# Performance work log

Measured on AMD Instinct MI355X. Metric: run time of the kernel, lower is better.

## Reference

```python
import jax, jax.numpy as jnp
import numpy as np

WIN = 9  # 9x9 local attention window

def conv2d(x, w, b=None, pad=1):
    # x: [B,C,H,W], w: [O,I,kh,kw]
    y = jax.lax.conv_general_dilated(x, w, (1, 1), [(pad, pad), (pad, pad)],
                                     dimension_numbers=('NCHW', 'OIHW', 'NCHW'))
    if b is not None:
        y = y + b[None, :, None, None]
    return y

def leaky(x):
    return jax.nn.leaky_relu(x, 0.2)

def local_similar(q, k):
    # TorchLocalAttention.f_similar: per-pixel dot(q[i,j], k[i+di-4, j+dj-4]) with zero pad,
    # kernel positions row-major (di*9+dj) -> output [B, 81, H, W]
    b, c, h, w = q.shape
    r = WIN // 2
    kp = jnp.pad(k, ((0, 0), (0, 0), (r, r), (r, r)))
    sims = []
    for di in range(WIN):
        for dj in range(WIN):
            sims.append(jnp.einsum('bchw,bchw->bhw', q, kp[:, :, di:di + h, dj:dj + w]))
    return jnp.stack(sims, axis=1)

def srp_forward(old, new, wq, bq, wk, bk, wv, bv, wo1, bo1, res_w1, res_w2, wo2, bo2):
    x = jnp.concatenate((old, new), axis=1)  # [B, C, H, W]
    att = local_similar(conv2d(x, wq, bq), conv2d(x, wk, bk))  # [B, 81, H, W]
    v = conv2d(att, wv, bv)  # [B, C, H, W]
    y = conv2d(x * v, wo1, bo1)
    n_res = res_w1.shape[0]
    for i in range(n_res):  # EBlock: ResBlocks (convs bias=False)
        h1 = leaky(conv2d(y, res_w1[i]))
        y = y + conv2d(h1, res_w2[i])
    y = conv2d(y, wo2, bo2)
    return y + x

def setup_inputs() -> dict:
    key = jax.random.key(0)
    B, Cn, Co, H, W = 4, 32, 32, 256, 256
    C = Cn + Co
    NRES = 8
    ks = jax.random.split(key, 16)
    s = 0.05
    inp = {
        'old': jax.random.normal(ks[0], (B, Co, H, W), jnp.float32),
        'new': jax.random.normal(ks[1], (B, Cn, H, W), jnp.float32),
        'wq': jax.random.normal(ks[2], (C, C, 3, 3), jnp.float32) * s,
        'bq': jax.random.normal(ks[3], (C,), jnp.float32) * s,
        'wk': jax.random.normal(ks[4], (C, C, 3, 3), jnp.float32) * s,
        'bk': jax.random.normal(ks[5], (C,), jnp.float32) * s,
        'wv': jax.random.normal(ks[6], (C, 81, 3, 3), jnp.float32) * s,
        'bv': jax.random.normal(ks[7], (C,), jnp.float32) * s,
        'wo1': jax.random.normal(ks[8], (C, C, 3, 3), jnp.float32) * s,
        'bo1': jax.random.normal(ks[9], (C,), jnp.float32) * s,
        'res_w1': jax.random.normal(ks[10], (NRES, C, C, 3, 3), jnp.float32) * s,
        'res_w2': jax.random.normal(ks[11], (NRES, C, C, 3, 3), jnp.float32) * s,
        'wo2': jax.random.normal(ks[12], (C, C, 3, 3), jnp.float32) * s,
        'bo2': jax.random.normal(ks[13], (C,), jnp.float32) * s,
    }
    return inp

def reference(old, new, wq, bq, wk, bk, wv, bv, wo1, bo1, res_w1, res_w2, wo2, bo2):
    return srp_forward(old, new, wq, bq, wk, bk, wv, bv, wo1, bo1, res_w1, res_w2, wo2, bo2)
```

## Files before the change

### kernel.cpp

```cpp
#include <hip/hip_runtime.h>
#include <hip/hip_bf16.h>


#define HH 256
#define WW 256
#define PLANE 65536

typedef _Float16 f16x8 __attribute__((ext_vector_type(8)));
typedef float    f32x4 __attribute__((ext_vector_type(4)));
typedef _Float16 h2    __attribute__((ext_vector_type(2)));

__device__ __forceinline__ unsigned short f2h(float f) {
    _Float16 h = (_Float16)f;
    return __builtin_bit_cast(unsigned short, h);
}
__device__ __forceinline__ float h2f(unsigned short u) {
    return (float)__builtin_bit_cast(_Float16, u);
}
__device__ __forceinline__ unsigned pack2h(float a, float b) {
    return (unsigned)f2h(a) | ((unsigned)f2h(b) << 16);
}
__device__ __forceinline__ float dot2h(unsigned a, unsigned b, float c) {
#if __has_builtin(__builtin_amdgcn_fdot2)
    return __builtin_amdgcn_fdot2(__builtin_bit_cast(h2, a),
                                  __builtin_bit_cast(h2, b), c, false);
#else
    h2 av = __builtin_bit_cast(h2, a), bv = __builtin_bit_cast(h2, b);
    return fmaf((float)av.x, (float)bv.x, fmaf((float)av.y, (float)bv.y, c));
#endif
}

__device__ __forceinline__ void gl16(const unsigned short* g, unsigned short* l) {
    __builtin_amdgcn_global_load_lds(
        (const __attribute__((address_space(1))) unsigned int*)(g),
        (__attribute__((address_space(3))) unsigned int*)(l),
        16, 0, 0);
}

template <int CIN, bool BIAS, bool LEAKY, bool ADDF, bool ADDX, bool MULX, bool OUTF, bool OUTB>
__global__ __launch_bounds__(256, 2) void conv_mfma(
    const unsigned short* __restrict__ in_pc,
    const unsigned short* __restrict__ wb,
    const float* __restrict__ bias,
    const unsigned short* __restrict__ addh,
    const unsigned short* __restrict__ xh,
    float* __restrict__ outf,
    unsigned short* __restrict__ outb)
{
    __shared__ unsigned short smem[39168];
    unsigned short* lds_w = smem + 20736;

    const int tid = threadIdx.x;
    const int w   = tid >> 6;
    const int ln  = tid & 63;
    const int m   = ln & 15;
    const int q   = ln >> 4;
    const int b   = blockIdx.z;
    const int tx0 = blockIdx.x * 16, ty0 = blockIdx.y * 16;
    const size_t pixb = (size_t)b * PLANE;
    const bool interior = (blockIdx.x >= 1) && (blockIdx.x <= 14) &&
                          (blockIdx.y >= 1) && (blockIdx.y <= 14);

    auto stage_in = [&](int c2s, unsigned short* dst) {
        if (interior) {
            const unsigned short* inb =
                in_pc + (pixb + (size_t)(ty0 - 1) * 256 + (tx0 - 1)) * CIN + c2s * 32;
#pragma unroll
            for (int it = 0; it < 5; ++it) {
                int u = it * 256 + tid;
                int pix = u >> 2, ps = u & 3;
                int part = ps ^ (pix & 3);
                int hy = pix / 18, hx = pix - hy * 18;
                gl16(inb + ((size_t)hy * 256 + hx) * CIN + part * 8,
                     &dst[(it * 256 + (tid & 192)) * 8]);
            }
            if (tid < 16) {
                int u = 1280 + tid;
                int pix = u >> 2, ps = u & 3;
                int part = ps ^ (pix & 3);
                int hy = pix / 18, hx = pix - hy * 18;
                gl16(inb + ((size_t)hy * 256 + hx) * CIN + part * 8,
                     &dst[1280 * 8]);
            }
        } else {
            for (int u = tid; u < 1296; u += 256) {
                int pix = u >> 2, part = u & 3;
                int hy = pix / 18, hx = pix - hy * 18;
                int gy = ty0 + hy - 1, gx = tx0 + hx - 1;
                uint4 val = make_uint4(0u, 0u, 0u, 0u);
                if ((unsigned)gy < 256u && (unsigned)gx < 256u)
                    val = *reinterpret_cast<const uint4*>(
                        in_pc + ((pixb + (size_t)gy * 256 + gx) * CIN + c2s * 32 + part * 8));
                *reinterpret_cast<uint4*>(&dst[pix * 32 + ((part ^ (pix & 3)) * 8)]) = val;
            }
        }
    };
    auto stage_w = [&](int c2s) {
        const int oc = tid >> 2, ps = tid & 3;
        const int part = ps ^ (oc & 3);
        const unsigned short* wsrc = wb + (size_t)oc * CIN + c2s * 32 + part * 8;
#pragma unroll
        for (int t = 0; t < 9; ++t)
            gl16(wsrc + (size_t)t * 64 * CIN,
                 &lds_w[t * 2048 + (tid & 192) * 8]);
    };

    f32x4 acc[4][4];
#pragma unroll
    for (int g = 0; g < 4; ++g)
#pragma unroll
        for (int p = 0; p < 4; ++p) acc[g][p] = (f32x4)0.f;

    constexpr int NC = CIN / 32;

    stage_in(0, smem);
    stage_w(0);
    __syncthreads();

    for (int c2 = 0; c2 < NC; ++c2) {
        unsigned short* cbuf = (c2 & 1) ? smem + 10368 : smem;
        if (c2 + 1 < NC)
            stage_in(c2 + 1, ((c2 + 1) & 1) ? smem + 10368 : smem);

#pragma unroll
        for (int t = 0; t < 9; ++t) {
            const int dy = t / 3, dx = t - dy * 3;
            f16x8 av[4], bv[4];
#pragma unroll
            for (int g = 0; g < 4; ++g) {
                int oc = g * 16 + m;
                av[g] = *reinterpret_cast<const f16x8*>(
                    &lds_w[t * 2048 + oc * 32 + ((q ^ (oc & 3)) * 8)]);
            }
#pragma unroll
            for (int p = 0; p < 4; ++p) {
                int hp = (w * 4 + p + dy) * 18 + m + dx;
                bv[p] = *reinterpret_cast<const f16x8*>(
                    &cbuf[hp * 32 + ((q ^ (hp & 3)) * 8)]);
            }
#pragma unroll
            for (int g = 0; g < 4; ++g)
#pragma unroll
                for (int p = 0; p < 4; ++p)
                    acc[g][p] = __builtin_amdgcn_mfma_f32_16x16x32_f16(
                        av[g], bv[p], acc[g][p], 0, 0, 0);
        }

        if (c2 + 1 < NC) {
            __syncthreads();
            stage_w(c2 + 1);
            __syncthreads();
        }
    }

    const int colx = tx0 + m;
    float4 bvec[4];
    if (BIAS) {
#pragma unroll
        for (int g = 0; g < 4; ++g)
            bvec[g] = *reinterpret_cast<const float4*>(bias + g * 16 + q * 4);
    }
    if (OUTB) __syncthreads();

#pragma unroll
    for (int g = 0; g < 4; ++g) {
#pragma unroll
        for (int p = 0; p < 4; ++p) {
            const int prow = w * 4 + p;
            const int gy   = ty0 + prow;
            const size_t pixg = pixb + (size_t)gy * 256 + colx;
            const int oc0 = g * 16 + q * 4;
            ushort4 a4, x4;
            if (ADDF) a4 = *reinterpret_cast<const ushort4*>(addh + pixg * 64 + oc0);
            if (ADDX || MULX) x4 = *reinterpret_cast<const ushort4*>(xh + pixg * 64 + oc0);
            float vals[4];
#pragma unroll
            for (int r = 0; r < 4; ++r) {
                float v = acc[g][p][r];
                if (BIAS) v += reinterpret_cast<const float*>(&bvec[g])[r];
                if (LEAKY) v = (v >= 0.f) ? v : 0.2f * v;
                if (ADDF) v += h2f(reinterpret_cast<const unsigned short*>(&a4)[r]);
                if (ADDX) v += h2f(reinterpret_cast<const unsigned short*>(&x4)[r]);
                if (MULX) v *= h2f(reinterpret_cast<const unsigned short*>(&x4)[r]);
                if (OUTF)
                    outf[((size_t)(b * 64 + oc0 + r)) * PLANE + (size_t)gy * 256 + colx] = v;
                vals[r] = v;
            }
            if (OUTB) {
                ushort4 pk;
                pk.x = f2h(vals[0]); pk.y = f2h(vals[1]);
                pk.z = f2h(vals[2]); pk.w = f2h(vals[3]);
                int pix   = prow * 16 + m;
                int part8 = g * 4 + q;
                int p16   = (part8 >> 1) ^ (pix & 7);
                *reinterpret_cast<ushort4*>(&smem[pix * 64 + p16 * 8 + (part8 & 1) * 4]) = pk;
            }
        }
    }
    if (OUTB) {
        __syncthreads();
        for (int u = tid; u < 2048; u += 256) {
            int pix = u >> 3, p16 = u & 7;
            uint4 val = *reinterpret_cast<const uint4*>(
                &smem[pix * 64 + ((p16 ^ (pix & 7)) * 8)]);
            int gy = ty0 + (pix >> 4), gx = tx0 + (pix & 15);
            *reinterpret_cast<uint4*>(
                &outb[(pixb + (size_t)gy * 256 + gx) * 64 + p16 * 8]) = val;
        }
    }
}

__global__ __launch_bounds__(256)
void local_sim(
    const unsigned short* __restrict__ qh, const unsigned short* __restrict__ kh,
    unsigned short* __restrict__ att)
{
    __shared__ unsigned short lds_k[576 * 64];

    const int tid = threadIdx.x;
    const int tx = tid & 15, ty = tid >> 4;
    const int bx = blockIdx.x * 16, by = blockIdx.y * 16;
    const int b  = blockIdx.z;
    const size_t pixb = (size_t)b * PLANE;
    const bool interior = (blockIdx.x >= 1) && (blockIdx.x <= 14) &&
                          (blockIdx.y >= 1) && (blockIdx.y <= 14);

    if (interior) {
        const unsigned short* kb =
            kh + (pixb + (size_t)(by - 4) * 256 + (bx - 4)) * 64;
#pragma unroll
        for (int it = 0; it < 18; ++it) {
            int u = it * 256 + tid;
            int pix = u >> 3, sl = u & 7;
            int part = sl ^ ((pix ^ (pix >> 3)) & 7);
            int hy = pix / 24, hx = pix - hy * 24;
            gl16(kb + ((size_t)hy * 256 + hx) * 64 + part * 8,
                 &lds_k[(it * 256 + (tid & 192)) * 8]);
        }
    } else {
        for (int u = tid; u < 4608; u += 256) {
            int pix = u >> 3, part = u & 7;
            int hy = pix / 24, hx = pix - hy * 24;
            int gy = by + hy - 4, gx = bx + hx - 4;
            uint4 val = make_uint4(0u, 0u, 0u, 0u);
            if ((unsigned)gy < 256u && (unsigned)gx < 256u)
                val = *reinterpret_cast<const uint4*>(
                    kh + ((pixb + (size_t)gy * 256 + gx) * 64 + part * 8));
            int sl = part ^ ((pix ^ (pix >> 3)) & 7);
            *reinterpret_cast<uint4*>(&lds_k[pix * 64 + sl * 8]) = val;
        }
    }
    __syncthreads();

    const unsigned short* qbase = qh + (pixb + (size_t)(by + ty) * 256 + bx + tx) * 64;
    unsigned short* op = att + (pixb + (size_t)(by + ty) * 256 + bx + tx) * 96;

    uint4 qv[8];
#pragma unroll
    for (int j = 0; j < 8; ++j)
        qv[j] = *reinterpret_cast<const uint4*>(qbase + j * 8);

#pragma unroll
    for (int g = 0; g < 3; ++g) {
        float acc[27];
#pragma unroll
        for (int i = 0; i < 27; ++i) acc[i] = 0.f;

#pragma unroll
        for (int dil = 0; dil < 3; ++dil) {
            const int hrow = (ty + g * 3 + dil) * 24 + tx;
#pragma unroll
            for (int dj = 0; dj < 9; ++dj) {
                const int hp = hrow + dj;
                const int gs = (hp ^ (hp >> 3)) & 7;
                float s = acc[dil * 9 + dj];
#pragma unroll
                for (int part = 0; part < 8; ++part) {
                    const uint4 kv = *reinterpret_cast<const uint4*>(
                        &lds_k[hp * 64 + ((part ^ gs) * 8)]);
                    s = dot2h(qv[part].x, kv.x, s);
                    s = dot2h(qv[part].y, kv.y, s);
                    s = dot2h(qv[part].z, kv.z, s);
                    s = dot2h(qv[part].w, kv.w, s);
                }
                acc[dil * 9 + dj] = s;
            }
        }

        unsigned short* o = op + g * 27;
        if (g == 0) {
            uint4 A = {pack2h(acc[0], acc[1]),  pack2h(acc[2], acc[3]),
                       pack2h(acc[4], acc[5]),  pack2h(acc[6], acc[7])};
            uint4 B = {pack2h(acc[8], acc[9]),  pack2h(acc[10], acc[11]),
                       pack2h(acc[12], acc[13]), pack2h(acc[14], acc[15])};
            uint2 C = {pack2h(acc[16], acc[17]), pack2h(acc[18], acc[19])};
            uint2 D = {pack2h(acc[20], acc[21]), pack2h(acc[22], acc[23])};
            *reinterpret_cast<uint4*>(o)      = A;
            *reinterpret_cast<uint4*>(o + 8)  = B;
            *reinterpret_cast<uint2*>(o + 16) = C;
            *reinterpret_cast<uint2*>(o + 20) = D;
            *reinterpret_cast<unsigned*>(o + 24) = pack2h(acc[24], acc[25]);
            o[26] = f2h(acc[26]);
        } else if (g == 1) {
            o[0] = f2h(acc[0]);
            *reinterpret_cast<unsigned*>(o + 1) = pack2h(acc[1], acc[2]);
            *reinterpret_cast<unsigned*>(o + 3) = pack2h(acc[3], acc[4]);
            uint4 A = {pack2h(acc[5], acc[6]),   pack2h(acc[7], acc[8]),
                       pack2h(acc[9], acc[10]),  pack2h(acc[11], acc[12])};
            uint4 B = {pack2h(acc[13], acc[14]), pack2h(acc[15], acc[16]),
                       pack2h(acc[17], acc[18]), pack2h(acc[19], acc[20])};
            *reinterpret_cast<uint4*>(o + 5)  = A;
            *reinterpret_cast<uint4*>(o + 13) = B;
            uint2 C = {pack2h(acc[21], acc[22]), pack2h(acc[23], acc[24])};
            *reinterpret_cast<uint2*>(o + 21) = C;
            *reinterpret_cast<unsigned*>(o + 25) = pack2h(acc[25], acc[26]);
        } else {
            *reinterpret_cast<unsigned*>(o) = pack2h(acc[0], acc[1]);
            uint4 A = {pack2h(acc[2], acc[3]),   pack2h(acc[4], acc[5]),
                       pack2h(acc[6], acc[7]),   pack2h(acc[8], acc[9])};
            uint4 B = {pack2h(acc[10], acc[11]), pack2h(acc[12], acc[13]),
                       pack2h(acc[14], acc[15]), pack2h(acc[16], acc[17])};
            *reinterpret_cast<uint4*>(o + 2)  = A;
            *reinterpret_cast<uint4*>(o + 10) = B;
            uint2 C = {pack2h(acc[18], acc[19]), pack2h(acc[20], acc[21])};
            *reinterpret_cast<uint2*>(o + 18) = C;
            *reinterpret_cast<unsigned*>(o + 22) = pack2h(acc[22], acc[23]);
            *reinterpret_cast<unsigned*>(o + 24) = pack2h(acc[24], acc[25]);
            o[26] = f2h(acc[26]);
        }
    }

    op[81] = 0;
    *reinterpret_cast<unsigned*>(op + 82) = 0u;
    uint2 z2 = {0u, 0u};
    uint4 z4 = {0u, 0u, 0u, 0u};
    *reinterpret_cast<uint2*>(op + 84) = z2;
    *reinterpret_cast<uint4*>(op + 88) = z4;
}

__global__ __launch_bounds__(256) void pack_x(
    const float* __restrict__ old_, const float* __restrict__ new_,
    unsigned short* __restrict__ xb)
{
    __shared__ unsigned short lds[256 * 64];
    const int tid = threadIdx.x;
    const int b = blockIdx.y;
    const size_t pixbase = (size_t)blockIdx.x * 256;
#pragma unroll
    for (int cg = 0; cg < 8; ++cg) {
        unsigned pk[4];
#pragma unroll
        for (int h = 0; h < 4; ++h) {
            int c0 = cg * 8 + h * 2;
            const float* s0 = (c0 < 32) ? old_ : new_;
            const float* s1 = ((c0 + 1) < 32) ? old_ : new_;
            float f0 = s0[((size_t)b * 32 + (c0 & 31)) * PLANE + pixbase + tid];
            float f1 = s1[((size_t)b * 32 + ((c0 + 1) & 31)) * PLANE + pixbase + tid];
            pk[h] = pack2h(f0, f1);
        }
        int p16 = cg ^ (tid & 7);
        uint4 v; v.x = pk[0]; v.y = pk[1]; v.z = pk[2]; v.w = pk[3];
        *reinterpret_cast<uint4*>(&lds[tid * 64 + p16 * 8]) = v;
    }
    __syncthreads();
    for (int r = 0; r < 8; ++r) {
        int u = r * 256 + tid;
        int pix = u >> 3, p16 = u & 7;
        uint4 v = *reinterpret_cast<const uint4*>(&lds[pix * 64 + ((p16 ^ (pix & 7)) * 8)]);
        *reinterpret_cast<uint4*>(
            &xb[((size_t)b * PLANE + pixbase + pix) * 64 + p16 * 8]) = v;
    }
}

__global__ void prep_wstd(const float* __restrict__ wq, const float* __restrict__ wk,
                          const float* __restrict__ wo1, const float* __restrict__ wo2,
                          const float* __restrict__ rw1, const float* __restrict__ rw2,
                          unsigned short* __restrict__ wstd)
{
    const int c = blockIdx.y;
    const float* src;
    if (c == 0) src = wq;
    else if (c == 1) src = wk;
    else if (c == 2) src = wo1;
    else if (c == 3) src = wo2;
    else if (c < 12) src = rw1 + (size_t)(c - 4) * 36864;
    else src = rw2 + (size_t)(c - 12) * 36864;
    int idx = blockIdx.x * 256 + threadIdx.x;
    int o = idx >> 6, i = idx & 63;
    const float* s = src + (size_t)(o * 64 + i) * 9;
    unsigned short* d = wstd + (size_t)c * 36864 + (size_t)o * 64 + i;
#pragma unroll
    for (int t = 0; t < 9; ++t) d[(size_t)t * 4096] = f2h(s[t]);
}

__global__ void prep_wv(const float* __restrict__ wv, unsigned short* __restrict__ wv96)
{
    int idx = blockIdx.x * 256 + threadIdx.x;
    int o = idx / 96, i = idx - o * 96;
    unsigned short* d = wv96 + (size_t)o * 96 + i;
    if (i < 81) {
        const float* s = wv + (size_t)(o * 81 + i) * 9;
#pragma unroll
        for (int t = 0; t < 9; ++t) d[(size_t)t * 6144] = f2h(s[t]);
    } else {
#pragma unroll
        for (int t = 0; t < 9; ++t) d[(size_t)t * 6144] = 0;
    }
}

extern "C" void kernel_launch(void* const* d_in, const int* in_sizes, int n_in,
                              void* d_out, int out_size, void* d_ws, size_t ws_size,
                              hipStream_t stream)
{
    const float* old_ = (const float*)d_in[0];
    const float* new_ = (const float*)d_in[1];
    const float* wq  = (const float*)d_in[2];  const float* bq  = (const float*)d_in[3];
    const float* wk  = (const float*)d_in[4];  const float* bk  = (const float*)d_in[5];
    const float* wv  = (const float*)d_in[6];  const float* bv  = (const float*)d_in[7];
    const float* wo1 = (const float*)d_in[8];  const float* bo1 = (const float*)d_in[9];
    const float* rw1 = (const float*)d_in[10]; const float* rw2 = (const float*)d_in[11];
    const float* wo2 = (const float*)d_in[12]; const float* bo2 = (const float*)d_in[13];
    float* out = (float*)d_out;

    char* ws = (char*)d_ws;
    unsigned short* X   = (unsigned short*)(ws);
    unsigned short* P1  = (unsigned short*)(ws + 33554432ull);
    unsigned short* P2  = (unsigned short*)(ws + 67108864ull);
    unsigned short* P3  = (unsigned short*)(ws + 100663296ull);
    unsigned short* wst = (unsigned short*)(ws + 150994944ull);
    unsigned short* wv96= (unsigned short*)(ws + 152469504ull);

    const dim3 cgrid(16, 16, 4), cblk(256);

    prep_wstd<<<dim3(16, 20), 256, 0, stream>>>(wq, wk, wo1, wo2, rw1, rw2, wst);
    prep_wv<<<dim3(24), 256, 0, stream>>>(wv, wv96);
    pack_x<<<dim3(256, 4), 256, 0, stream>>>(old_, new_, X);

    conv_mfma<64, true, false, false, false, false, false, true>
        <<<cgrid, cblk, 0, stream>>>(X, wst + 0ull * 36864, bq, nullptr, nullptr, nullptr, P1);
    conv_mfma<64, true, false, false, false, false, false, true>
        <<<cgrid, cblk, 0, stream>>>(X, wst + 1ull * 36864, bk, nullptr, nullptr, nullptr, P2);
    local_sim<<<cgrid, cblk, 0, stream>>>(P1, P2, P3);
    conv_mfma<96, true, false, false, false, true, false, true>
        <<<cgrid, cblk, 0, stream>>>(P3, wv96, bv, nullptr, X, nullptr, P2);
    conv_mfma<64, true, false, false, false, false, false, true>
        <<<cgrid, cblk, 0, stream>>>(P2, wst + 2ull * 36864, bo1, nullptr, nullptr, nullptr, P1);
    for (int i = 0; i < 8; ++i) {
        unsigned short* ysrc = (i & 1) ? P3 : P1;
        unsigned short* ydst = (i & 1) ? P1 : P3;
        conv_mfma<64, false, true, false, false, false, false, true>
            <<<cgrid, cblk, 0, stream>>>(ysrc, wst + (size_t)(4 + i) * 36864, nullptr,
                                         nullptr, nullptr, nullptr, P2);
        conv_mfma<64, false, false, true, false, false, false, true>
            <<<cgrid, cblk, 0, stream>>>(P2, wst + (size_t)(12 + i) * 36864, nullptr,
                                         ysrc, nullptr, nullptr, ydst);
    }
    conv_mfma<64, true, false, false, true, false, true, false>
        <<<cgrid, cblk, 0, stream>>>(P1, wst + 3ull * 36864, bo2, nullptr, X, out, nullptr);
}
```

Measured before the change: 833.3 us.

## Stage full 64-channel input tile once and double-buffer weights by tap pairs

For 64-input-channel convolutions, the kernel now loads the whole 18x18x64 halo tile into LDS at once with an 8-way XOR swizzle. It then streams weights in chunks of two taps through two LDS buffers, so the next chunk loads while MFMAs run on the current one. This replaces the old two-pass channel split, which needed two barriers plus a serial weight reload per pass. In exchange there are five barrier rounds per tile and a different LDS layout, and the final barrier moves inside the loop.

```diff
diff --git a/kernel.cpp b/kernel.cpp
--- a/kernel.cpp
+++ b/kernel.cpp
@@ -48,7 +48,6 @@
     unsigned short* __restrict__ outb)
 {
     __shared__ unsigned short smem[39168];
-    unsigned short* lds_w = smem + 20736;
 
     const int tid = threadIdx.x;
     const int w   = tid >> 6;
@@ -61,96 +60,189 @@
     const bool interior = (blockIdx.x >= 1) && (blockIdx.x <= 14) &&
                           (blockIdx.y >= 1) && (blockIdx.y <= 14);
 
-    auto stage_in = [&](int c2s, unsigned short* dst) {
+    f32x4 acc[4][4];
+#pragma unroll
+    for (int g = 0; g < 4; ++g)
+#pragma unroll
+        for (int p = 0; p < 4; ++p) acc[g][p] = (f32x4)0.f;
+
+    if constexpr (CIN == 64) {
+        unsigned short* lds_in = smem;
+        unsigned short* wbuf0  = smem + 20736;
+        unsigned short* wbuf1  = smem + 28928;
+
         if (interior) {
             const unsigned short* inb =
-                in_pc + (pixb + (size_t)(ty0 - 1) * 256 + (tx0 - 1)) * CIN + c2s * 32;
-#pragma unroll
-            for (int it = 0; it < 5; ++it) {
+                in_pc + (pixb + (size_t)(ty0 - 1) * 256 + (tx0 - 1)) * 64;
+#pragma unroll
+            for (int it = 0; it < 10; ++it) {
                 int u = it * 256 + tid;
-                int pix = u >> 2, ps = u & 3;
-                int part = ps ^ (pix & 3);
+                int pix = u >> 3, ps = u & 7;
+                int part = ps ^ (pix & 7);
                 int hy = pix / 18, hx = pix - hy * 18;
-                gl16(inb + ((size_t)hy * 256 + hx) * CIN + part * 8,
-                     &dst[(it * 256 + (tid & 192)) * 8]);
-            }
-            if (tid < 16) {
-                int u = 1280 + tid;
-                int pix = u >> 2, ps = u & 3;
-                int part = ps ^ (pix & 3);
+                gl16(inb + ((size_t)hy * 256 + hx) * 64 + part * 8,
+                     &lds_in[(it * 256 + (tid & 192)) * 8]);
+            }
+            if (tid < 32) {
+                int u = 2560 + tid;
+                int pix = u >> 3, ps = u & 7;
+                int part = ps ^ (pix & 7);
                 int hy = pix / 18, hx = pix - hy * 18;
-                gl16(inb + ((size_t)hy * 256 + hx) * CIN + part * 8,
-                     &dst[1280 * 8]);
+                gl16(inb + ((size_t)hy * 256 + hx) * 64 + part * 8,
+                     &lds_in[2560 * 8]);
             }
         } else {
-            for (int u = tid; u < 1296; u += 256) {
-                int pix = u >> 2, part = u & 3;
+            for (int u = tid; u < 2592; u += 256) {
+                int pix = u >> 3, part = u & 7;
                 int hy = pix / 18, hx = pix - hy * 18;
                 int gy = ty0 + hy - 1, gx = tx0 + hx - 1;
                 uint4 val = make_uint4(0u, 0u, 0u, 0u);
                 if ((unsigned)gy < 256u && (unsigned)gx < 256u)
                     val = *reinterpret_cast<const uint4*>(
-                        in_pc + ((pixb + (size_t)gy * 256 + gx) * CIN + c2s * 32 + part * 8));
-                *reinterpret_cast<uint4*>(&dst[pix * 32 + ((part ^ (pix & 3)) * 8)]) = val;
-            }
-        }
-    };
-    auto stage_w = [&](int c2s) {
-        const int oc = tid >> 2, ps = tid & 3;
-        const int part = ps ^ (oc & 3);
-        const unsigned short* wsrc = wb + (size_t)oc * CIN + c2s * 32 + part * 8;
-#pragma unroll
-        for (int t = 0; t < 9; ++t)
-            gl16(wsrc + (size_t)t * 64 * CIN,
-                 &lds_w[t * 2048 + (tid & 192) * 8]);
-    };
-
-    f32x4 acc[4][4];
-#pragma unroll
-    for (int g = 0; g < 4; ++g)
-#pragma unroll
-        for (int p = 0; p < 4; ++p) acc[g][p] = (f32x4)0.f;
-
-    constexpr int NC = CIN / 32;
-
-    stage_in(0, smem);
-    stage_w(0);
-    __syncthreads();
-
-    for (int c2 = 0; c2 < NC; ++c2) {
-        unsigned short* cbuf = (c2 & 1) ? smem + 10368 : smem;
-        if (c2 + 1 < NC)
-            stage_in(c2 + 1, ((c2 + 1) & 1) ? smem + 10368 : smem);
-
-#pragma unroll
-        for (int t = 0; t < 9; ++t) {
-            const int dy = t / 3, dx = t - dy * 3;
-            f16x8 av[4], bv[4];
-#pragma unroll
-            for (int g = 0; g < 4; ++g) {
-                int oc = g * 16 + m;
-                av[g] = *reinterpret_cast<const f16x8*>(
-                    &lds_w[t * 2048 + oc * 32 + ((q ^ (oc & 3)) * 8)]);
-            }
-#pragma unroll
-            for (int p = 0; p < 4; ++p) {
-                int hp = (w * 4 + p + dy) * 18 + m + dx;
-                bv[p] = *reinterpret_cast<const f16x8*>(
-                    &cbuf[hp * 32 + ((q ^ (hp & 3)) * 8)]);
-            }
-#pragma unroll
-            for (int g = 0; g < 4; ++g)
-#pragma unroll
-                for (int p = 0; p < 4; ++p)
-                    acc[g][p] = __builtin_amdgcn_mfma_f32_16x16x32_f16(
-                        av[g], bv[p], acc[g][p], 0, 0, 0);
-        }
-
-        if (c2 + 1 < NC) {
+                        in_pc + ((pixb + (size_t)gy * 256 + gx) * 64 + part * 8));
+                int sl = part ^ (pix & 7);
+                *reinterpret_cast<uint4*>(&lds_in[pix * 64 + sl * 8]) = val;
+            }
+        }
+
+        auto stage_w = [&](int t0, int ntaps, unsigned short* dst) {
+            for (int it = 0; it < ntaps * 2; ++it) {
+                int u = it * 256 + tid;
+                int row = u >> 3, sl = u & 7;
+                int part = sl ^ (row & 7);
+                gl16(wb + ((size_t)((t0 + (row >> 6)) * 64 + (row & 63))) * 64 + part * 8,
+                     &dst[(it * 256 + (tid & 192)) * 8]);
+            }
+        };
+
+        stage_w(0, 2, wbuf0);
+        __syncthreads();
+
+#pragma unroll
+        for (int gi = 0; gi < 5; ++gi) {
+            const int t0 = gi * 2;
+            const int nt = (gi == 4) ? 1 : 2;
+            unsigned short* cw = (gi & 1) ? wbuf1 : wbuf0;
+            if (gi < 4)
+                stage_w((gi + 1) * 2, (gi + 1 == 4) ? 1 : 2, (gi & 1) ? wbuf0 : wbuf1);
+
+#pragma unroll
+            for (int tl = 0; tl < nt; ++tl) {
+                const int t = t0 + tl;
+                const int dy = t / 3, dx = t - dy * 3;
+#pragma unroll
+                for (int c2 = 0; c2 < 2; ++c2) {
+                    f16x8 av[4], bv[4];
+#pragma unroll
+                    for (int g = 0; g < 4; ++g) {
+                        int row = tl * 64 + g * 16 + m;
+                        av[g] = *reinterpret_cast<const f16x8*>(
+                            &cw[row * 64 + (((c2 * 4 + q) ^ (m & 7)) * 8)]);
+                    }
+#pragma unroll
+                    for (int p = 0; p < 4; ++p) {
+                        int hp = (w * 4 + p + dy) * 18 + m + dx;
+                        bv[p] = *reinterpret_cast<const f16x8*>(
+                            &lds_in[hp * 64 + (((c2 * 4 + q) ^ (hp & 7)) * 8)]);
+                    }
+#pragma unroll
+                    for (int g = 0; g < 4; ++g)
+#pragma unroll
+                        for (int p = 0; p < 4; ++p)
+                            acc[g][p] = __builtin_amdgcn_mfma_f32_16x16x32_f16(
+                                av[g], bv[p], acc[g][p], 0, 0, 0);
+                }
+            }
             __syncthreads();
-            stage_w(c2 + 1);
-            __syncthreads();
-        }
+        }
+    } else {
+        unsigned short* lds_w = smem + 20736;
+
+        auto stage_in = [&](int c2s, unsigned short* dst) {
+            if (interior) {
+                const unsigned short* inb =
+                    in_pc + (pixb + (size_t)(ty0 - 1) * 256 + (tx0 - 1)) * CIN + c2s * 32;
+#pragma unroll
+                for (int it = 0; it < 5; ++it) {
+                    int u = it * 256 + tid;
+                    int pix = u >> 2, ps = u & 3;
+                    int part = ps ^ (pix & 3);
+                    int hy = pix / 18, hx = pix - hy * 18;
+                    gl16(inb + ((size_t)hy * 256 + hx) * CIN + part * 8,
+                         &dst[(it * 256 + (tid & 192)) * 8]);
+                }
+                if (tid < 16) {
+                    int u = 1280 + tid;
+                    int pix = u >> 2, ps = u & 3;
+                    int part = ps ^ (pix & 3);
+                    int hy = pix / 18, hx = pix - hy * 18;
+                    gl16(inb + ((size_t)hy * 256 + hx) * CIN + part * 8,
+                         &dst[1280 * 8]);
+                }
+            } else {
+                for (int u = tid; u < 1296; u += 256) {
+                    int pix = u >> 2, part = u & 3;
+                    int hy = pix / 18, hx = pix - hy * 18;
+                    int gy = ty0 + hy - 1, gx = tx0 + hx - 1;
+                    uint4 val = make_uint4(0u, 0u, 0u, 0u);
+                    if ((unsigned)gy < 256u && (unsigned)gx < 256u)
+                        val = *reinterpret_cast<const uint4*>(
+                            in_pc + ((pixb + (size_t)gy * 256 + gx) * CIN + c2s * 32 + part * 8));
+                    *reinterpret_cast<uint4*>(&dst[pix * 32 + ((part ^ (pix & 3)) * 8)]) = val;
+                }
+            }
+        };
+        auto stage_w = [&](int c2s) {
+            const int oc = tid >> 2, ps = tid & 3;
+            const int part = ps ^ (oc & 3);
+            const unsigned short* wsrc = wb + (size_t)oc * CIN + c2s * 32 + part * 8;
+#pragma unroll
+            for (int t = 0; t < 9; ++t)
+                gl16(wsrc + (size_t)t * 64 * CIN,
+                     &lds_w[t * 2048 + (tid & 192) * 8]);
+        };
+
+        constexpr int NC = CIN / 32;
+        stage_in(0, smem);
+        stage_w(0);
+        __syncthreads();
+
+        for (int c2 = 0; c2 < NC; ++c2) {
+            unsigned short* cbuf = (c2 & 1) ? smem + 10368 : smem;
+            if (c2 + 1 < NC)
+                stage_in(c2 + 1, ((c2 + 1) & 1) ? smem + 10368 : smem);
+
+#pragma unroll
+            for (int t = 0; t < 9; ++t) {
+                const int dy = t / 3, dx = t - dy * 3;
+                f16x8 av[4], bv[4];
+#pragma unroll
+                for (int g = 0; g < 4; ++g) {
+                    int oc = g * 16 + m;
+                    av[g] = *reinterpret_cast<const f16x8*>(
+                        &lds_w[t * 2048 + oc * 32 + ((q ^ (oc & 3)) * 8)]);
+                }
+#pragma unroll
+                for (int p = 0; p < 4; ++p) {
+                    int hp = (w * 4 + p + dy) * 18 + m + dx;
+                    bv[p] = *reinterpret_cast<const f16x8*>(
+                        &cbuf[hp * 32 + ((q ^ (hp & 3)) * 8)]);
+                }
+#pragma unroll
+                for (int g = 0; g < 4; ++g)
+#pragma unroll
+                    for (int p = 0; p < 4; ++p)
+                        acc[g][p] = __builtin_amdgcn_mfma_f32_16x16x32_f16(
+                            av[g], bv[p], acc[g][p], 0, 0, 0);
+            }
+
+            if (c2 + 1 < NC) {
+                __syncthreads();
+                stage_w(c2 + 1);
+                __syncthreads();
+            }
+        }
+        if (OUTB) __syncthreads();
     }
 
     const int colx = tx0 + m;
@@ -160,7 +252,6 @@
         for (int g = 0; g < 4; ++g)
             bvec[g] = *reinterpret_cast<const float4*>(bias + g * 16 + q * 4);
     }
-    if (OUTB) __syncthreads();
 
 #pragma unroll
     for (int g = 0; g < 4; ++g) {
```

After: 839.5 us. Within noise of the previous version (+0.7%).

## Fuse each ResBlock's two 3x3 convs into one kernel with halo recompute

Applied to the files above, without the earlier changes.

Adds a res_fused kernel that computes the first conv plus leaky ReLU on an 18x18 halo tile, keeps the intermediate in LDS, then runs the second conv and the residual add, writing y directly. The two per-ResBlock launches are replaced by one. This removes the global write and re-read of the intermediate activation and halves the launch count for the residual stack. The cost is about 27% redundant MFMA work for the halo, higher LDS use per block, and less overlap because staging is no longer double-buffered.

```diff
diff --git a/kernel.cpp b/kernel.cpp
--- a/kernel.cpp
+++ b/kernel.cpp
@@ -112,7 +112,6 @@
         for (int p = 0; p < 4; ++p) acc[g][p] = (f32x4)0.f;
 
     constexpr int NC = CIN / 32;
-
     stage_in(0, smem);
     stage_w(0);
     __syncthreads();
@@ -207,6 +206,212 @@
             *reinterpret_cast<uint4*>(
                 &outb[(pixb + (size_t)gy * 256 + gx) * 64 + p16 * 8]) = val;
         }
+    }
+}
+
+__global__ __launch_bounds__(256, 2) void res_fused(
+    const unsigned short* __restrict__ yin,
+    const unsigned short* __restrict__ w1,
+    const unsigned short* __restrict__ w2,
+    unsigned short* __restrict__ yout)
+{
+    __shared__ unsigned short smem[39168];
+    unsigned short* lds_w = smem + 20736;
+
+    const int tid = threadIdx.x;
+    const int w   = tid >> 6;
+    const int ln  = tid & 63;
+    const int m   = ln & 15;
+    const int q   = ln >> 4;
+    const int b   = blockIdx.z;
+    const int tx0 = blockIdx.x * 16, ty0 = blockIdx.y * 16;
+    const size_t pixb = (size_t)b * PLANE;
+    const bool interior = (blockIdx.x >= 1) && (blockIdx.x <= 14) &&
+                          (blockIdx.y >= 1) && (blockIdx.y <= 14);
+
+    int jr[6], jc[6];
+#pragma unroll
+    for (int j = 0; j < 6; ++j) {
+        int g = (j < 5) ? (w + 4 * j) : 20;
+        int pix = g * 16 + m;
+        jr[j] = pix / 18;
+        jc[j] = pix - jr[j] * 18;
+    }
+
+    auto stage_y = [&](int c2s) {
+        if (interior) {
+            const unsigned short* inb =
+                yin + (pixb + (size_t)(ty0 - 2) * 256 + (tx0 - 2)) * 64 + c2s * 32;
+#pragma unroll
+            for (int it = 0; it < 6; ++it) {
+                int u = it * 256 + tid;
+                int pix = u >> 2, ps = u & 3;
+                int part = ps ^ (pix & 3);
+                int hy = pix / 20, hx = pix - hy * 20;
+                gl16(inb + ((size_t)hy * 256 + hx) * 64 + part * 8,
+                     &smem[(it * 256 + (tid & 192)) * 8]);
+            }
+            if (tid < 64) {
+                int u = 1536 + tid;
+                int pix = u >> 2, ps = u & 3;
+                int part = ps ^ (pix & 3);
+                int hy = pix / 20, hx = pix - hy * 20;
+                gl16(inb + ((size_t)hy * 256 + hx) * 64 + part * 8,
+                     &smem[1536 * 8]);
+            }
+        } else {
+            for (int u = tid; u < 1600; u += 256) {
+                int pix = u >> 2, part = u & 3;
+                int hy = pix / 20, hx = pix - hy * 20;
+                int gy = ty0 + hy - 2, gx = tx0 + hx - 2;
+                uint4 val = make_uint4(0u, 0u, 0u, 0u);
+                if ((unsigned)gy < 256u && (unsigned)gx < 256u)
+                    val = *reinterpret_cast<const uint4*>(
+                        yin + ((pixb + (size_t)gy * 256 + gx) * 64 + c2s * 32 + part * 8));
+                *reinterpret_cast<uint4*>(&smem[pix * 32 + ((part ^ (pix & 3)) * 8)]) = val;
+            }
+        }
+    };
+    auto stage_w = [&](const unsigned short* wsrcb, int c2s) {
+        const int oc = tid >> 2, ps = tid & 3;
+        const int part = ps ^ (oc & 3);
+        const unsigned short* wsrc = wsrcb + (size_t)oc * 64 + c2s * 32 + part * 8;
+#pragma unroll
+        for (int t = 0; t < 9; ++t)
+            gl16(wsrc + (size_t)t * 64 * 64, &lds_w[t * 2048 + (tid & 192) * 8]);
+    };
+
+    f32x4 acc1[6][4];
+#pragma unroll
+    for (int j = 0; j < 6; ++j)
+#pragma unroll
+        for (int g4 = 0; g4 < 4; ++g4) acc1[j][g4] = (f32x4)0.f;
+
+    for (int c2 = 0; c2 < 2; ++c2) {
+        if (c2) __syncthreads();
+        stage_y(c2);
+        stage_w(w1, c2);
+        __syncthreads();
+
+#pragma unroll
+        for (int t = 0; t < 9; ++t) {
+            const int dy = t / 3, dx = t - dy * 3;
+            f16x8 av[4];
+#pragma unroll
+            for (int g4 = 0; g4 < 4; ++g4) {
+                int oc = g4 * 16 + m;
+                av[g4] = *reinterpret_cast<const f16x8*>(
+                    &lds_w[t * 2048 + oc * 32 + ((q ^ (oc & 3)) * 8)]);
+            }
+#pragma unroll
+            for (int j = 0; j < 6; ++j) {
+                int ypix = (jr[j] + dy) * 20 + jc[j] + dx;
+                f16x8 bv = *reinterpret_cast<const f16x8*>(
+                    &smem[ypix * 32 + ((q ^ (ypix & 3)) * 8)]);
+#pragma unroll
+                for (int g4 = 0; g4 < 4; ++g4)
+                    acc1[j][g4] = __builtin_amdgcn_mfma_f32_16x16x32_f16(
+                        av[g4], bv, acc1[j][g4], 0, 0, 0);
+            }
+        }
+    }
+
+    __syncthreads();
+    stage_w(w2, 0);
+#pragma unroll
+    for (int j = 0; j < 6; ++j) {
+        const int g = (j < 5) ? (w + 4 * j) : 20;
+        const int pix = g * 16 + m;
+        const bool wr = (j < 5) || (w == 0 && m < 4);
+        const int gy = ty0 - 1 + jr[j], gx = tx0 - 1 + jc[j];
+        const bool ok = ((unsigned)gy < 256u) && ((unsigned)gx < 256u);
+        if (wr) {
+#pragma unroll
+            for (int g4 = 0; g4 < 4; ++g4) {
+                ushort4 pk;
+#pragma unroll
+                for (int r = 0; r < 4; ++r) {
+                    float v = acc1[j][g4][r];
+                    v = (v >= 0.f) ? v : 0.2f * v;
+                    reinterpret_cast<unsigned short*>(&pk)[r] = ok ? f2h(v) : (unsigned short)0;
+                }
+                int part8 = g4 * 2 + (q >> 1);
+                *reinterpret_cast<ushort4*>(
+                    &smem[pix * 64 + ((part8 ^ (pix & 7)) * 8) + (q & 1) * 4]) = pk;
+            }
+        }
+    }
+    __syncthreads();
+
+    f32x4 acc2[4][4];
+#pragma unroll
+    for (int g4 = 0; g4 < 4; ++g4)
+#pragma unroll
+        for (int p = 0; p < 4; ++p) acc2[g4][p] = (f32x4)0.f;
+
+    for (int c2 = 0; c2 < 2; ++c2) {
+        if (c2) {
+            __syncthreads();
+            stage_w(w2, 1);
+            __syncthreads();
+        }
+#pragma unroll
+        for (int t = 0; t < 9; ++t) {
+            const int dy = t / 3, dx = t - dy * 3;
+            f16x8 av[4], bv[4];
+#pragma unroll
+            for (int g4 = 0; g4 < 4; ++g4) {
+                int oc = g4 * 16 + m;
+                av[g4] = *reinterpret_cast<const f16x8*>(
+                    &lds_w[t * 2048 + oc * 32 + ((q ^ (oc & 3)) * 8)]);
+            }
+#pragma unroll
+            for (int p = 0; p < 4; ++p) {
+                int hp = (w * 4 + p + dy) * 18 + m + dx;
+                bv[p] = *reinterpret_cast<const f16x8*>(
+                    &smem[hp * 64 + (((c2 * 4 + q) ^ (hp & 7)) * 8)]);
+            }
+#pragma unroll
+            for (int g4 = 0; g4 < 4; ++g4)
+#pragma unroll
+                for (int p = 0; p < 4; ++p)
+                    acc2[g4][p] = __builtin_amdgcn_mfma_f32_16x16x32_f16(
+                        av[g4], bv[p], acc2[g4][p], 0, 0, 0);
+        }
+    }
+
+    __syncthreads();
+    const int colx = tx0 + m;
+#pragma unroll
+    for (int g4 = 0; g4 < 4; ++g4) {
+#pragma unroll
+        for (int p = 0; p < 4; ++p) {
+            const int prow = w * 4 + p;
+            const int gy   = ty0 + prow;
+            const size_t pixg = pixb + (size_t)gy * 256 + colx;
+            const int oc0 = g4 * 16 + q * 4;
+            ushort4 a4 = *reinterpret_cast<const ushort4*>(yin + pixg * 64 + oc0);
+            ushort4 pk;
+#pragma unroll
+            for (int r = 0; r < 4; ++r) {
+                float v = acc2[g4][p][r] +
+                          h2f(reinterpret_cast<const unsigned short*>(&a4)[r]);
+                reinterpret_cast<unsigned short*>(&pk)[r] = f2h(v);
+            }
+            int pix   = prow * 16 + m;
+            int part8 = g4 * 4 + q;
+            int p16   = (part8 >> 1) ^ (pix & 7);
+            *reinterpret_cast<ushort4*>(&smem[pix * 64 + p16 * 8 + (part8 & 1) * 4]) = pk;
+        }
+    }
+    __syncthreads();
+    for (int u = tid; u < 2048; u += 256) {
+        int pix = u >> 3, p16 = u & 7;
+        uint4 val = *reinterpret_cast<const uint4*>(
+            &smem[pix * 64 + ((p16 ^ (pix & 7)) * 8)]);
+        int gy = ty0 + (pix >> 4), gx = tx0 + (pix & 15);
+        *reinterpret_cast<uint4*>(
+            &yout[(pixb + (size_t)gy * 256 + gx) * 64 + p16 * 8]) = val;
     }
 }
 
@@ -448,12 +653,8 @@
     for (int i = 0; i < 8; ++i) {
         unsigned short* ysrc = (i & 1) ? P3 : P1;
         unsigned short* ydst = (i & 1) ? P1 : P3;
-        conv_mfma<64, false, true, false, false, false, false, true>
-            <<<cgrid, cblk, 0, stream>>>(ysrc, wst + (size_t)(4 + i) * 36864, nullptr,
-                                         nullptr, nullptr, nullptr, P2);
-        conv_mfma<64, false, false, true, false, false, false, true>
-            <<<cgrid, cblk, 0, stream>>>(P2, wst + (size_t)(12 + i) * 36864, nullptr,
-                                         ysrc, nullptr, nullptr, ydst);
+        res_fused<<<cgrid, cblk, 0, stream>>>(
+            ysrc, wst + (size_t)(4 + i) * 36864, wst + (size_t)(12 + i) * 36864, ydst);
     }
     conv_mfma<64, true, false, false, true, false, true, false>
         <<<cgrid, cblk, 0, stream>>>(P1, wst + 3ull * 36864, bo2, nullptr, X, out, nullptr);
```

New measurement: 795.7 us. -4.5%, faster.
